# Kernel optimization log

Hardware: AMD Instinct MI355X
Metric: run time of the kernel (lower is better)

## Reference

```python
import jax, jax.numpy as jnp
import numpy as np

DN = ('NCHW', 'OIHW', 'NCHW')

def _conv(x, W, pad):
    return jax.lax.conv_general_dilated(x, W, (1, 1), [(pad, pad), (pad, pad)], dimension_numbers=DN)

def _cbs(x, W, s, b, pad):
    # Conv2d(bias=False) + folded BatchNorm (scale/bias) + SiLU
    y = _conv(x, W, pad) * s[None, :, None, None] + b[None, :, None, None]
    return y * jax.nn.sigmoid(y)

def _l2norm(x):
    n = jnp.sqrt(jnp.sum(x * x, axis=1, keepdims=True))
    return x / jnp.maximum(n, 1e-12)

def setup_inputs() -> dict:
    key = jax.random.key(0)
    ks = jax.random.split(key, 24)
    B, C, H, L, TD, NC = 16, 256, 64, 40, 768, 8
    EMB = (TD + NC * 2) // 2  # 392
    w = lambda k, sh: jax.random.normal(k, sh, jnp.float32) * 0.02
    img = jax.random.normal(ks[0], (B, C, H, H), jnp.float32)
    flang = jax.random.normal(ks[1], (B, L, TD), jnp.float32)
    lengths = jax.random.randint(ks[2], (B, 1), 5, L + 1)
    word_mask = (jnp.arange(L)[None, :] < lengths).astype(jnp.int32)
    return {
        'img': img, 'flang': flang, 'word_mask': word_mask, 'sigma_w': 0.1,
        'W1': w(ks[3], (EMB, TD)), 'b1': w(ks[4], (EMB,)),
        'W2': w(ks[5], (NC * 2, EMB)), 'b2': w(ks[6], (NC * 2,)),
        'Wv': w(ks[7], (C, C, 1, 1)), 'sv': jnp.ones((C,)), 'bv': w(ks[8], (C,)),
        'Wg': w(ks[9], (NC, NC, 1, 1)), 'sg': jnp.ones((NC,)), 'bg': w(ks[10], (NC,)),
        'Wb': w(ks[11], (NC, NC, 1, 1)), 'sb': jnp.ones((NC,)), 'bb': w(ks[12], (NC,)),
        'Wf1': w(ks[13], (C, C, 1, 1)), 'sf1': jnp.ones((C,)), 'bf1': w(ks[14], (C,)),
        'Wf2': w(ks[15], (C, C, 3, 3)), 'sf2': jnp.ones((C,)), 'bf2': w(ks[16], (C,)),
        'Wf3': w(ks[17], (C, C, 1, 1)), 'bf3': w(ks[18], (C,)),
        'Ws': w(ks[19], (NC, C, 3, 3)), 'bs': w(ks[20], (NC,)),
        'add_weight': jnp.zeros((), jnp.float32),
    }

def reference(img, flang, word_mask, sigma_w, W1, b1, W2, b2, Wv, sv, bv,
              Wg, sg, bg, Wb, sb, bb, Wf1, sf1, bf1, Wf2, sf2, bf2,
              Wf3, bf3, Ws, bs, add_weight):
    B, C, H = img.shape[0], img.shape[1], img.shape[2]
    nc = Wg.shape[0]
    map_visu = jnp.tanh(_cbs(img, Wv, sv, bv, 0))
    # ragged masked mean excluding first (CLS) and last (SEP) masked tokens
    m = word_mask.astype(jnp.float32)
    c = jnp.cumsum(m, axis=1)
    tot = c[:, -1:]
    inc = m * ((c > 1) & (c < tot)).astype(jnp.float32)  # [B,L]
    flang_avg = jnp.sum(flang * inc[:, :, None], axis=1) / jnp.sum(inc, axis=1, keepdims=True)
    map_flang = jax.nn.sigmoid((flang_avg @ W1.T + b1) @ W2.T + b2)  # [B,2*nc]
    maps = map_flang.reshape(B, nc, 2)
    sigma_x = sigma_w * H
    sig = _conv(img, Ws, 0) + bs[None, :, None, None]  # [B,nc,H-2,H-2]
    sigma_weight = jax.nn.sigmoid(jnp.mean(sig, axis=(2, 3), keepdims=True))  # [B,nc,1,1]
    sigma_y = sigma_x * sigma_weight
    yc = (maps[:, :, 0] * H).astype(jnp.int32).astype(jnp.float32)[:, :, None, None]
    xc = (maps[:, :, 1] * H).astype(jnp.int32).astype(jnp.float32)[:, :, None, None]
    gy = jnp.arange(H, dtype=jnp.float32)[None, None, :, None]
    gx = jnp.arange(H, dtype=jnp.float32)[None, None, None, :]
    weights = jnp.exp(-((gy - yc) ** 2 / (2.0 * sigma_y ** 2) + (gx - xc) ** 2 / (2.0 * sigma_x ** 2)))  # [B,nc,H,H]
    gamma = jnp.tanh(_cbs(weights, Wg, sg, bg, 0))
    beta = jnp.tanh(_cbs(weights, Wb, sb, bb, 0))
    g = jnp.mean(gamma, axis=1, keepdims=True)
    bmax = jnp.max(beta, axis=1, keepdims=True)
    v_film = _l2norm(g * map_visu + bmax)
    v_film = _cbs(v_film, Wf1, sf1, bf1, 0)
    v_film = _cbs(v_film, Wf2, sf2, bf2, 1)
    v_film = _conv(v_film, Wf3, 0) + bf3[None, :, None, None]
    aw = jnp.tanh(add_weight)
    v_add = (1.0 + aw) * img + (1.0 - aw) * v_film
    return _l2norm(v_add)
```

## Files before the change

### kernel.cpp

```cpp
#include <hip/hip_runtime.h>
#include <hip/hip_bf16.h>


#define DEVFN static __device__ __forceinline__

DEVFN float sigmoidf_(float x) { return 1.f / (1.f + expf(-x)); }
DEVFN float siluf_(float y) { return y / (1.f + expf(-y)); }

typedef __attribute__((ext_vector_type(8))) short bf16x8;
typedef __attribute__((ext_vector_type(4))) float f32x4;

DEVFN unsigned short f2bf_(float f) {
    union { __hip_bfloat16 b; unsigned short u; } cv;
    cv.b = __float2bfloat16(f);
    return cv.u;
}

__global__ void prep_kernel(const float* __restrict__ Wv, const float* __restrict__ Wf1,
                            const float* __restrict__ Wf3, const float* __restrict__ Wf2,
                            short* __restrict__ WvB, short* __restrict__ W1B,
                            short* __restrict__ W3B, short* __restrict__ WB2) {
    int idx = blockIdx.x * 256 + threadIdx.x;
    if (idx < 65536) {
        int j    = idx & 7;
        int lane = (idx >> 3) & 63;
        int coT  = (idx >> 9) & 15;
        int ci32 = (idx >> 13) & 7;
        int co = coT * 16 + (lane & 15);
        int ci = ci32 * 32 + ((lane >> 4) << 3) + j;
        int src = co * 256 + ci;
        WvB[idx] = (short)f2bf_(Wv[src]);
        W1B[idx] = (short)f2bf_(Wf1[src]);
        W3B[idx] = (short)f2bf_(Wf3[src]);
    }
    int o = idx - 65536;
    if (o >= 0 && o < 589824) {
        int j    = o & 7;
        int lane = (o >> 3) & 63;
        int coT  = (o >> 9) & 15;
        int ci32 = (o >> 13) & 7;
        int kk   = o >> 16;
        int co = coT * 16 + (lane & 15);
        int ci = ci32 * 32 + ((lane >> 4) << 3) + j;
        WB2[o] = (short)f2bf_(Wf2[(co * 256 + ci) * 9 + kk]);
    }
}

__global__ void lang_kernel(const float* __restrict__ flang, const int* __restrict__ mask,
                            float* __restrict__ fa) {
    __shared__ float inc[40];
    __shared__ float isum;
    int b = blockIdx.x, t = threadIdx.x;
    if (t == 0) {
        float cum[40];
        float c = 0.f;
        for (int l = 0; l < 40; ++l) { c += (float)mask[b * 40 + l]; cum[l] = c; }
        float tot = c, s = 0.f;
        for (int l = 0; l < 40; ++l) {
            float m = (float)mask[b * 40 + l];
            float v = (cum[l] > 1.f && cum[l] < tot) ? m : 0.f;
            inc[l] = v; s += v;
        }
        isum = s;
    }
    __syncthreads();
    for (int d = t; d < 768; d += 256) {
        float a = 0.f;
        for (int l = 0; l < 40; ++l) a += flang[(size_t)(b * 40 + l) * 768 + d] * inc[l];
        fa[b * 768 + d] = a / isum;
    }
}

__global__ void mlp_kernel(const float* __restrict__ fa_g, const float* __restrict__ W1,
                           const float* __restrict__ b1, const float* __restrict__ W2,
                           const float* __restrict__ b2, float* __restrict__ ycxc) {
    __shared__ float fa[768];
    __shared__ float h[392];
    __shared__ float o[16];
    int b = blockIdx.x, t = threadIdx.x;
    for (int k = t; k < 768; k += 448) fa[k] = fa_g[b * 768 + k];
    __syncthreads();
    if (t < 392) {
        float a = b1[t];
        const float* w = W1 + (size_t)t * 768;
        for (int k = 0; k < 768; ++k) a = fmaf(fa[k], w[k], a);
        h[t] = a;
    }
    __syncthreads();
    if (t < 16) {
        float a = b2[t];
        const float* w = W2 + (size_t)t * 392;
        for (int k = 0; k < 392; ++k) a = fmaf(h[k], w[k], a);
        o[t] = sigmoidf_(a);
    }
    __syncthreads();
    if (t < 8) {
        ycxc[b * 8 + t]       = (float)(int)(o[2 * t] * 64.f);
        ycxc[128 + b * 8 + t] = (float)(int)(o[2 * t + 1] * 64.f);
    }
}

__global__ void wsum_kernel(const float* __restrict__ img, float* __restrict__ S) {
    __shared__ float red[9 * 256];
    int bc = blockIdx.x;
    int t = threadIdx.x;
    float s[9];
#pragma unroll
    for (int k = 0; k < 9; ++k) s[k] = 0.f;
    const float* p = img + (size_t)bc * 4096;
    for (int j = 0; j < 16; ++j) {
        int idx = t + j * 256;
        int y = idx >> 6, x = idx & 63;
        float v = p[idx];
#pragma unroll
        for (int ky = 0; ky < 3; ++ky) {
            if (y < ky || y > ky + 61) continue;
#pragma unroll
            for (int kx = 0; kx < 3; ++kx) {
                if (x < kx || x > kx + 61) continue;
                s[ky * 3 + kx] += v;
            }
        }
    }
#pragma unroll
    for (int k = 0; k < 9; ++k) red[k * 256 + t] = s[k];
    __syncthreads();
    for (int st = 128; st > 0; st >>= 1) {
        if (t < st) {
#pragma unroll
            for (int k = 0; k < 9; ++k) red[k * 256 + t] += red[k * 256 + t + st];
        }
        __syncthreads();
    }
    if (t < 9) S[(size_t)bc * 9 + t] = red[t * 256];
}

__global__ void sigw_kernel(const float* __restrict__ Ws, const float* __restrict__ S,
                            const float* __restrict__ bs, float* __restrict__ sigw) {
    __shared__ float red[8 * 256];
    int b = blockIdx.x, t = threadIdx.x;
    float sv[9];
    const float* Sp = S + (size_t)(b * 256 + t) * 9;
#pragma unroll
    for (int k = 0; k < 9; ++k) sv[k] = Sp[k];
#pragma unroll
    for (int co = 0; co < 8; ++co) {
        const float* wp = Ws + (size_t)(co * 256 + t) * 9;
        float a = 0.f;
#pragma unroll
        for (int k = 0; k < 9; ++k) a = fmaf(wp[k], sv[k], a);
        red[co * 256 + t] = a;
    }
    __syncthreads();
    for (int st = 128; st > 0; st >>= 1) {
        if (t < st) {
#pragma unroll
            for (int co = 0; co < 8; ++co) red[co * 256 + t] += red[co * 256 + t + st];
        }
        __syncthreads();
    }
    if (t < 8) sigw[b * 8 + t] = sigmoidf_(red[t * 256] / 3844.f + bs[t]);
}

__global__ void gauss_kernel(const float* __restrict__ ycxc, const float* __restrict__ sigw,
                             const float* __restrict__ sigma_w,
                             const float* __restrict__ Wg, const float* __restrict__ sg,
                             const float* __restrict__ bg,
                             const float* __restrict__ Wb, const float* __restrict__ sb,
                             const float* __restrict__ bb,
                             float* __restrict__ g, float* __restrict__ bm) {
    int blk = blockIdx.x;
    int b = blk >> 6, y = blk & 63;
    int x = threadIdx.x;
    float sx = sigma_w[0] * 64.f;
    float w[8];
#pragma unroll
    for (int n = 0; n < 8; ++n) {
        float yc = ycxc[b * 8 + n], xc = ycxc[128 + b * 8 + n];
        float sy = sx * sigw[b * 8 + n];
        float dy = (float)y - yc, dx = (float)x - xc;
        w[n] = expf(-(dy * dy / (2.f * sy * sy) + dx * dx / (2.f * sx * sx)));
    }
    float gacc = 0.f, bmax = -3.4e38f;
#pragma unroll
    for (int n = 0; n < 8; ++n) {
        float a1 = 0.f, a2 = 0.f;
#pragma unroll
        for (int m = 0; m < 8; ++m) {
            a1 = fmaf(Wg[n * 8 + m], w[m], a1);
            a2 = fmaf(Wb[n * 8 + m], w[m], a2);
        }
        float ga = tanhf(siluf_(a1 * sg[n] + bg[n]));
        float be = tanhf(siluf_(a2 * sb[n] + bb[n]));
        gacc += ga;
        bmax = fmaxf(bmax, be);
    }
    g[(size_t)(b * 64 + y) * 64 + x] = gacc * 0.125f;
    bm[(size_t)(b * 64 + y) * 64 + x] = bmax;
}

__global__ __launch_bounds__(256) void f01_kernel(
        const float* __restrict__ img, const short* __restrict__ wvb,
        const short* __restrict__ w1b,
        const float* __restrict__ sv, const float* __restrict__ bv,
        const float* __restrict__ s1, const float* __restrict__ b1,
        const float* __restrict__ g, const float* __restrict__ bm,
        __hip_bfloat16* __restrict__ outB) {
    __shared__ __attribute__((aligned(16))) short lA[64 * 264];
    __shared__ float invs[64];
    __shared__ float ls_sv[256], ls_bv[256], ls_s1[256], ls_b1[256];
    __shared__ float ls_g[64], ls_bm[64];
    float* pr = (float*)lA;
    int blk = blockIdx.x, b = blk >> 6, y = blk & 63;
    int t = threadIdx.x, w = t >> 6, lane = t & 63;
    int lx = lane & 15, koct = lane >> 4;

    ls_sv[t] = sv[t]; ls_bv[t] = bv[t];
    ls_s1[t] = s1[t]; ls_b1[t] = b1[t];
    if (t < 64) {
        ls_g[t]  = g[(size_t)(b * 64 + y) * 64 + t];
        ls_bm[t] = bm[(size_t)(b * 64 + y) * 64 + t];
    }

    {
        int x = t & 63, cg = t >> 6;
        const float* ib = img + (size_t)b * 1048576 + y * 64 + x;
#pragma unroll
        for (int c8 = 0; c8 < 8; ++c8) {
            int ci0 = cg * 64 + c8 * 8;
            unsigned short r[8];
#pragma unroll
            for (int j = 0; j < 8; ++j) r[j] = f2bf_(ib[(size_t)(ci0 + j) * 4096]);
            *(uint4*)&lA[x * 264 + ci0] = *(uint4*)r;
        }
    }
    f32x4 acc[4][4];
#pragma unroll
    for (int mi = 0; mi < 4; ++mi)
#pragma unroll
        for (int ni = 0; ni < 4; ++ni) acc[mi][ni] = (f32x4){0.f, 0.f, 0.f, 0.f};
    __syncthreads();

#pragma unroll
    for (int k32 = 0; k32 < 8; ++k32) {
        const short* wp = wvb + (((k32 * 16) + w * 4) * 64 + lane) * 8;
        bf16x8 bfr[4];
#pragma unroll
        for (int ni = 0; ni < 4; ++ni) bfr[ni] = *(const bf16x8*)(wp + ni * 512);
        bf16x8 afr[4];
#pragma unroll
        for (int mi = 0; mi < 4; ++mi)
            afr[mi] = *(const bf16x8*)&lA[(mi * 16 + lx) * 264 + k32 * 32 + koct * 8];
#pragma unroll
        for (int mi = 0; mi < 4; ++mi)
#pragma unroll
            for (int ni = 0; ni < 4; ++ni)
                acc[mi][ni] = __builtin_amdgcn_mfma_f32_16x16x32_bf16(afr[mi], bfr[ni], acc[mi][ni], 0, 0, 0);
    }
    __syncthreads();

#pragma unroll
    for (int mi = 0; mi < 4; ++mi)
#pragma unroll
        for (int rr = 0; rr < 4; ++rr) {
            int x = mi * 16 + koct * 4 + rr;
            float ps = 0.f;
#pragma unroll
            for (int ni = 0; ni < 4; ++ni) {
                int co = w * 64 + ni * 16 + lx;
                float yv = fmaf(acc[mi][ni][rr], ls_sv[co], ls_bv[co]);
                float mvv = tanhf(siluf_(yv));
                float v = fmaf(ls_g[x], mvv, ls_bm[x]);
                acc[mi][ni][rr] = v;
                ps += v * v;
            }
            pr[x * 64 + w * 16 + lx] = ps;
        }
    __syncthreads();
    if (t < 64) {
        float s2 = 0.f;
        for (int q = 0; q < 64; ++q) s2 += pr[t * 64 + q];
        invs[t] = 1.f / fmaxf(sqrtf(s2), 1e-12f);
    }
    __syncthreads();

#pragma unroll
    for (int mi = 0; mi < 4; ++mi)
#pragma unroll
        for (int ni = 0; ni < 4; ++ni) {
            int co = w * 64 + ni * 16 + lx;
#pragma unroll
            for (int rr = 0; rr < 4; ++rr) {
                int x = mi * 16 + koct * 4 + rr;
                lA[x * 264 + co] = (short)f2bf_(acc[mi][ni][rr] * invs[x]);
            }
        }
#pragma unroll
    for (int mi = 0; mi < 4; ++mi)
#pragma unroll
        for (int ni = 0; ni < 4; ++ni) acc[mi][ni] = (f32x4){0.f, 0.f, 0.f, 0.f};
    __syncthreads();

#pragma unroll
    for (int k32 = 0; k32 < 8; ++k32) {
        const short* wp = w1b + (((k32 * 16) + w * 4) * 64 + lane) * 8;
        bf16x8 bfr[4];
#pragma unroll
        for (int ni = 0; ni < 4; ++ni) bfr[ni] = *(const bf16x8*)(wp + ni * 512);
        bf16x8 afr[4];
#pragma unroll
        for (int mi = 0; mi < 4; ++mi)
            afr[mi] = *(const bf16x8*)&lA[(mi * 16 + lx) * 264 + k32 * 32 + koct * 8];
#pragma unroll
        for (int mi = 0; mi < 4; ++mi)
#pragma unroll
            for (int ni = 0; ni < 4; ++ni)
                acc[mi][ni] = __builtin_amdgcn_mfma_f32_16x16x32_bf16(afr[mi], bfr[ni], acc[mi][ni], 0, 0, 0);
    }
    __syncthreads();

#pragma unroll
    for (int mi = 0; mi < 4; ++mi)
#pragma unroll
        for (int ni = 0; ni < 4; ++ni) {
            int co = w * 64 + ni * 16 + lx;
#pragma unroll
            for (int rr = 0; rr < 4; ++rr) {
                int x = mi * 16 + koct * 4 + rr;
                float yv = fmaf(acc[mi][ni][rr], ls_s1[co], ls_b1[co]);
                lA[x * 264 + co] = (short)f2bf_(siluf_(yv));
            }
        }
    __syncthreads();
    unsigned short* og = (unsigned short*)outB + (size_t)(b * 64 + y) * 16384;
#pragma unroll
    for (int it = 0; it < 8; ++it) {
        int e8 = t + it * 256;
        int x2 = e8 >> 5, c8 = e8 & 31;
        *(uint4*)(og + e8 * 8) = *(uint4*)&lA[x2 * 264 + c8 * 8];
    }
}

__global__ __launch_bounds__(256, 2) void conv3x3_mfma(const __hip_bfloat16* __restrict__ xin,
                                                       const short* __restrict__ wb,
                                                       const float* __restrict__ sc,
                                                       const float* __restrict__ bi,
                                                       __hip_bfloat16* __restrict__ outB) {
    __shared__ __attribute__((aligned(16))) short lds[4 * 66 * 72];
    int blk = blockIdx.x;
    int b = blk >> 5, y0 = (blk & 31) * 2;
    int t = threadIdx.x;
    int w = t >> 6, lane = t & 63;
    int lx = lane & 15, koct = lane >> 4;
    const unsigned short* xg = (const unsigned short*)xin + (size_t)b * 1048576;

    f32x4 acc[8][4];
#pragma unroll
    for (int mi = 0; mi < 8; ++mi)
#pragma unroll
        for (int ni = 0; ni < 4; ++ni) acc[mi][ni] = (f32x4){0.f, 0.f, 0.f, 0.f};

    for (int cc = 0; cc < 4; ++cc) {
        __syncthreads();
#pragma unroll
        for (int p = 0; p < 9; ++p) {
            int u = t + p * 256;
            if (u < 2112) {
                int r = u / 528;
                int rem = u - r * 528;
                int xp = rem >> 3, ci8 = rem & 7;
                int ys = y0 + r - 1, xs = xp - 1;
                uint4 v = {0u, 0u, 0u, 0u};
                if (ys >= 0 && ys < 64 && xs >= 0 && xs < 64)
                    v = *(const uint4*)(xg + ((size_t)(ys * 64 + xs) * 256 + cc * 64 + ci8 * 8));
                *(uint4*)&lds[(r * 66 + xp) * 72 + ci8 * 8] = v;
            }
        }
        __syncthreads();
        for (int kk = 0; kk < 9; ++kk) {
            int ky = kk / 3, kx = kk - ky * 3;
#pragma unroll
            for (int k32 = 0; k32 < 2; ++k32) {
                int ci32g = cc * 2 + k32;
                const short* wp = wb + ((((kk * 8 + ci32g) * 16) + w * 4) * 64 + lane) * 8;
                bf16x8 bfr[4];
#pragma unroll
                for (int ni = 0; ni < 4; ++ni)
                    bfr[ni] = *(const bf16x8*)(wp + ni * 512);
                bf16x8 afr[8];
#pragma unroll
                for (int mi = 0; mi < 8; ++mi) {
                    int row = mi >> 2, xb = (mi & 3) * 16;
                    afr[mi] = *(const bf16x8*)&lds[((row + ky) * 66 + xb + lx + kx) * 72 + k32 * 32 + koct * 8];
                }
#pragma unroll
                for (int mi = 0; mi < 8; ++mi)
#pragma unroll
                    for (int ni = 0; ni < 4; ++ni)
                        acc[mi][ni] = __builtin_amdgcn_mfma_f32_16x16x32_bf16(afr[mi], bfr[ni], acc[mi][ni], 0, 0, 0);
            }
        }
    }
#pragma unroll
    for (int r2 = 0; r2 < 2; ++r2) {
        __syncthreads();
#pragma unroll
        for (int mi4 = 0; mi4 < 4; ++mi4) {
            int mi = r2 * 4 + mi4;
#pragma unroll
            for (int ni = 0; ni < 4; ++ni) {
                int co = w * 64 + ni * 16 + lx;
                float s = sc[co], bb2 = bi[co];
#pragma unroll
                for (int rr = 0; rr < 4; ++rr) {
                    int x = mi4 * 16 + koct * 4 + rr;
                    float yv = fmaf(acc[mi][ni][rr], s, bb2);
                    lds[x * 264 + co] = (short)f2bf_(siluf_(yv));
                }
            }
        }
        __syncthreads();
        unsigned short* og = (unsigned short*)outB + (size_t)(b * 64 + y0 + r2) * 16384;
#pragma unroll
        for (int it = 0; it < 8; ++it) {
            int e8 = t + it * 256;
            int x2 = e8 >> 5, c8 = e8 & 31;
            *(uint4*)(og + e8 * 8) = *(uint4*)&lds[x2 * 264 + c8 * 8];
        }
    }
}

__global__ __launch_bounds__(256) void final_mfma(const __hip_bfloat16* __restrict__ inB,
                                                  const short* __restrict__ w3b,
                                                  const float* __restrict__ bf3,
                                                  const float* __restrict__ img,
                                                  const float* __restrict__ addw,
                                                  float* __restrict__ outF) {
    __shared__ __attribute__((aligned(16))) short lA[64 * 264];
    __shared__ float invs[64];
    __shared__ float ls_b[256];
    float* pr = (float*)lA;
    int blk = blockIdx.x, b = blk >> 6, y = blk & 63;
    int t = threadIdx.x, w = t >> 6, lane = t & 63;
    int lx = lane & 15, koct = lane >> 4;
    ls_b[t] = bf3[t];

    const unsigned short* xg = (const unsigned short*)inB + (size_t)(b * 64 + y) * 16384;
#pragma unroll
    for (int it = 0; it < 8; ++it) {
        int e8 = t + it * 256;
        int x2 = e8 >> 5, c8 = e8 & 31;
        *(uint4*)&lA[x2 * 264 + c8 * 8] = *(const uint4*)(xg + e8 * 8);
    }
    f32x4 acc[4][4];
#pragma unroll
    for (int mi = 0; mi < 4; ++mi)
#pragma unroll
        for (int ni = 0; ni < 4; ++ni) acc[mi][ni] = (f32x4){0.f, 0.f, 0.f, 0.f};
    __syncthreads();

#pragma unroll
    for (int k32 = 0; k32 < 8; ++k32) {
        const short* wp = w3b + (((k32 * 16) + w * 4) * 64 + lane) * 8;
        bf16x8 bfr[4];
#pragma unroll
        for (int ni = 0; ni < 4; ++ni) bfr[ni] = *(const bf16x8*)(wp + ni * 512);
        bf16x8 afr[4];
#pragma unroll
        for (int mi = 0; mi < 4; ++mi)
            afr[mi] = *(const bf16x8*)&lA[(mi * 16 + lx) * 264 + k32 * 32 + koct * 8];
#pragma unroll
        for (int mi = 0; mi < 4; ++mi)
#pragma unroll
            for (int ni = 0; ni < 4; ++ni)
                acc[mi][ni] = __builtin_amdgcn_mfma_f32_16x16x32_bf16(afr[mi], bfr[ni], acc[mi][ni], 0, 0, 0);
    }
    __syncthreads();

    float aw = tanhf(addw[0]);
#pragma unroll
    for (int mi = 0; mi < 4; ++mi)
#pragma unroll
        for (int ni = 0; ni < 4; ++ni) {
            int co = w * 64 + ni * 16 + lx;
            const float* ip = img + ((size_t)(b * 256 + co) * 64 + y) * 64 + mi * 16 + koct * 4;
            float4 im = *(const float4*)ip;
            float imv[4] = {im.x, im.y, im.z, im.w};
#pragma unroll
            for (int rr = 0; rr < 4; ++rr) {
                float v = (1.f + aw) * imv[rr] + (1.f - aw) * (acc[mi][ni][rr] + ls_b[co]);
                acc[mi][ni][rr] = v;
            }
        }
#pragma unroll
    for (int mi = 0; mi < 4; ++mi)
#pragma unroll
        for (int rr = 0; rr < 4; ++rr) {
            int x = mi * 16 + koct * 4 + rr;
            float ps = 0.f;
#pragma unroll
            for (int ni = 0; ni < 4; ++ni) ps += acc[mi][ni][rr] * acc[mi][ni][rr];
            pr[x * 64 + w * 16 + lx] = ps;
        }
    __syncthreads();
    if (t < 64) {
        float s2 = 0.f;
        for (int q = 0; q < 64; ++q) s2 += pr[t * 64 + q];
        invs[t] = 1.f / fmaxf(sqrtf(s2), 1e-12f);
    }
    __syncthreads();
#pragma unroll
    for (int mi = 0; mi < 4; ++mi)
#pragma unroll
        for (int ni = 0; ni < 4; ++ni) {
            int co = w * 64 + ni * 16 + lx;
            float r[4];
#pragma unroll
            for (int rr = 0; rr < 4; ++rr) {
                int x = mi * 16 + koct * 4 + rr;
                r[rr] = acc[mi][ni][rr] * invs[x];
            }
            float* op = outF + ((size_t)(b * 256 + co) * 64 + y) * 64 + mi * 16 + koct * 4;
            *(float4*)op = *(float4*)r;
        }
}

extern "C" void kernel_launch(void* const* d_in, const int* in_sizes, int n_in,
                              void* d_out, int out_size, void* d_ws, size_t ws_size,
                              hipStream_t stream) {
    const float* img     = (const float*)d_in[0];
    const float* flang   = (const float*)d_in[1];
    const int*   wmask   = (const int*)d_in[2];
    const float* sigma_w = (const float*)d_in[3];
    const float* W1      = (const float*)d_in[4];
    const float* b1      = (const float*)d_in[5];
    const float* W2      = (const float*)d_in[6];
    const float* b2      = (const float*)d_in[7];
    const float* Wv      = (const float*)d_in[8];
    const float* sv      = (const float*)d_in[9];
    const float* bv      = (const float*)d_in[10];
    const float* Wg      = (const float*)d_in[11];
    const float* sg      = (const float*)d_in[12];
    const float* bg      = (const float*)d_in[13];
    const float* Wb      = (const float*)d_in[14];
    const float* sb      = (const float*)d_in[15];
    const float* bb      = (const float*)d_in[16];
    const float* Wf1     = (const float*)d_in[17];
    const float* sf1     = (const float*)d_in[18];
    const float* bf1     = (const float*)d_in[19];
    const float* Wf2     = (const float*)d_in[20];
    const float* sf2     = (const float*)d_in[21];
    const float* bf2     = (const float*)d_in[22];
    const float* Wf3     = (const float*)d_in[23];
    const float* bf3     = (const float*)d_in[24];
    const float* Ws      = (const float*)d_in[25];
    const float* bs      = (const float*)d_in[26];
    const float* addw    = (const float*)d_in[27];
    float* out = (float*)d_out;
    float* ws  = (float*)d_ws;

    short* WvB  = (short*)ws;
    short* W1B  = (short*)(ws + 32768);
    short* W3B  = (short*)(ws + 65536);
    short* WB2  = (short*)(ws + 98304);
    float* fa   = ws + 393216;
    float* ycxc = ws + 405504;
    float* S    = ws + 405760;
    float* sigw = ws + 442624;
    float* gmap = ws + 442752;
    float* bmap = ws + 508288;
    __hip_bfloat16* bufA = (__hip_bfloat16*)(ws + 573824);
    __hip_bfloat16* bufB = (__hip_bfloat16*)(ws + 8962432);

    prep_kernel<<<2560, 256, 0, stream>>>(Wv, Wf1, Wf3, Wf2, WvB, W1B, W3B, WB2);
    lang_kernel<<<16, 256, 0, stream>>>(flang, wmask, fa);
    mlp_kernel<<<16, 448, 0, stream>>>(fa, W1, b1, W2, b2, ycxc);
    wsum_kernel<<<4096, 256, 0, stream>>>(img, S);
    sigw_kernel<<<16, 256, 0, stream>>>(Ws, S, bs, sigw);
    gauss_kernel<<<1024, 64, 0, stream>>>(ycxc, sigw, sigma_w, Wg, sg, bg, Wb, sb, bb, gmap, bmap);
    f01_kernel<<<1024, 256, 0, stream>>>(img, WvB, W1B, sv, bv, sf1, bf1, gmap, bmap, bufB);
    conv3x3_mfma<<<512, 256, 0, stream>>>(bufB, WB2, sf2, bf2, bufA);
    final_mfma<<<1024, 256, 0, stream>>>(bufA, W3B, bf3, img, addw, out);
}
```

Measured before the change: 430.0 us.

## Prefetch next conv3x3 channel chunk into registers; restructure final kernel epilogue

The 3x3 conv kernel now precomputes load offsets and register-prefetches the next 64-channel input chunk while MFMAs run on the current one, hiding global-load latency behind compute. The final 1x1 kernel stages conv output through LDS as bf16 in a channel-major layout and recomputes the residual-plus-l2norm with coalesced per-pixel img reads and output writes. It also raises its occupancy hint. tanh and SiLU switch to fast-exp approximations. The bf16 staging of the final conv output and the fast math add rounding error, and the extra prefetch registers may raise register pressure.

```diff
diff --git a/kernel.cpp b/kernel.cpp
--- a/kernel.cpp
+++ b/kernel.cpp
@@ -5,7 +5,8 @@
 #define DEVFN static __device__ __forceinline__
 
 DEVFN float sigmoidf_(float x) { return 1.f / (1.f + expf(-x)); }
-DEVFN float siluf_(float y) { return y / (1.f + expf(-y)); }
+DEVFN float siluf_(float y) { return y / (1.f + __expf(-y)); }
+DEVFN float tanh_fast_(float x) { return 1.f - 2.f / (__expf(2.f * x) + 1.f); }
 
 typedef __attribute__((ext_vector_type(8))) short bf16x8;
 typedef __attribute__((ext_vector_type(4))) float f32x4;
@@ -14,6 +15,11 @@
     union { __hip_bfloat16 b; unsigned short u; } cv;
     cv.b = __float2bfloat16(f);
     return cv.u;
+}
+DEVFN float bf2f_(unsigned short u) {
+    union { unsigned short u; __hip_bfloat16 b; } cv;
+    cv.u = u;
+    return __bfloat162float(cv.b);
 }
 
 __global__ void prep_kernel(const float* __restrict__ Wv, const float* __restrict__ Wf1,
@@ -269,7 +275,7 @@
             for (int ni = 0; ni < 4; ++ni) {
                 int co = w * 64 + ni * 16 + lx;
                 float yv = fmaf(acc[mi][ni][rr], ls_sv[co], ls_bv[co]);
-                float mvv = tanhf(siluf_(yv));
+                float mvv = tanh_fast_(siluf_(yv));
                 float v = fmaf(ls_g[x], mvv, ls_bm[x]);
                 acc[mi][ni][rr] = v;
                 ps += v * v;
@@ -354,35 +360,54 @@
     int lx = lane & 15, koct = lane >> 4;
     const unsigned short* xg = (const unsigned short*)xin + (size_t)b * 1048576;
 
+    int goff[9], loff[9];
+    bool uval[9], uin[9];
+#pragma unroll
+    for (int p = 0; p < 9; ++p) {
+        int u = t + p * 256;
+        uval[p] = (u < 2112);
+        int r = u / 528;
+        int rem = u - r * 528;
+        int xp = rem >> 3, ci8 = rem & 7;
+        int ys = y0 + r - 1, xs = xp - 1;
+        uin[p] = uval[p] && ys >= 0 && ys < 64 && xs >= 0 && xs < 64;
+        goff[p] = (ys * 64 + xs) * 256 + ci8 * 8;
+        loff[p] = (r * 66 + xp) * 72 + ci8 * 8;
+    }
+    uint4 pf[9];
+
     f32x4 acc[8][4];
 #pragma unroll
     for (int mi = 0; mi < 8; ++mi)
 #pragma unroll
         for (int ni = 0; ni < 4; ++ni) acc[mi][ni] = (f32x4){0.f, 0.f, 0.f, 0.f};
 
+#pragma unroll
+    for (int p = 0; p < 9; ++p) {
+        uint4 v = {0u, 0u, 0u, 0u};
+        if (uin[p]) v = *(const uint4*)(xg + goff[p]);
+        pf[p] = v;
+    }
+#pragma unroll
+    for (int p = 0; p < 9; ++p)
+        if (uval[p]) *(uint4*)&lds[loff[p]] = pf[p];
+    __syncthreads();
+
     for (int cc = 0; cc < 4; ++cc) {
-        __syncthreads();
-#pragma unroll
-        for (int p = 0; p < 9; ++p) {
-            int u = t + p * 256;
-            if (u < 2112) {
-                int r = u / 528;
-                int rem = u - r * 528;
-                int xp = rem >> 3, ci8 = rem & 7;
-                int ys = y0 + r - 1, xs = xp - 1;
+        if (cc < 3) {
+#pragma unroll
+            for (int p = 0; p < 9; ++p) {
                 uint4 v = {0u, 0u, 0u, 0u};
-                if (ys >= 0 && ys < 64 && xs >= 0 && xs < 64)
-                    v = *(const uint4*)(xg + ((size_t)(ys * 64 + xs) * 256 + cc * 64 + ci8 * 8));
-                *(uint4*)&lds[(r * 66 + xp) * 72 + ci8 * 8] = v;
-            }
-        }
-        __syncthreads();
+                if (uin[p]) v = *(const uint4*)(xg + goff[p] + (cc + 1) * 64);
+                pf[p] = v;
+            }
+        }
+#pragma unroll
         for (int kk = 0; kk < 9; ++kk) {
             int ky = kk / 3, kx = kk - ky * 3;
 #pragma unroll
             for (int k32 = 0; k32 < 2; ++k32) {
-                int ci32g = cc * 2 + k32;
-                const short* wp = wb + ((((kk * 8 + ci32g) * 16) + w * 4) * 64 + lane) * 8;
+                const short* wp = wb + ((((kk * 8 + cc * 2 + k32) * 16) + w * 4) * 64 + lane) * 8;
                 bf16x8 bfr[4];
 #pragma unroll
                 for (int ni = 0; ni < 4; ++ni)
@@ -400,10 +425,16 @@
                         acc[mi][ni] = __builtin_amdgcn_mfma_f32_16x16x32_bf16(afr[mi], bfr[ni], acc[mi][ni], 0, 0, 0);
             }
         }
+        __syncthreads();
+        if (cc < 3) {
+#pragma unroll
+            for (int p = 0; p < 9; ++p)
+                if (uval[p]) *(uint4*)&lds[loff[p]] = pf[p];
+            __syncthreads();
+        }
     }
 #pragma unroll
     for (int r2 = 0; r2 < 2; ++r2) {
-        __syncthreads();
 #pragma unroll
         for (int mi4 = 0; mi4 < 4; ++mi4) {
             int mi = r2 * 4 + mi4;
@@ -427,19 +458,20 @@
             int x2 = e8 >> 5, c8 = e8 & 31;
             *(uint4*)(og + e8 * 8) = *(uint4*)&lds[x2 * 264 + c8 * 8];
         }
-    }
-}
-
-__global__ __launch_bounds__(256) void final_mfma(const __hip_bfloat16* __restrict__ inB,
-                                                  const short* __restrict__ w3b,
-                                                  const float* __restrict__ bf3,
-                                                  const float* __restrict__ img,
-                                                  const float* __restrict__ addw,
-                                                  float* __restrict__ outF) {
+        __syncthreads();
+    }
+}
+
+__global__ __launch_bounds__(256, 4) void final_mfma(const __hip_bfloat16* __restrict__ inB,
+                                                     const short* __restrict__ w3b,
+                                                     const float* __restrict__ bf3,
+                                                     const float* __restrict__ img,
+                                                     const float* __restrict__ addw,
+                                                     float* __restrict__ outF) {
     __shared__ __attribute__((aligned(16))) short lA[64 * 264];
+    __shared__ float pr2[256];
     __shared__ float invs[64];
     __shared__ float ls_b[256];
-    float* pr = (float*)lA;
     int blk = blockIdx.x, b = blk >> 6, y = blk & 63;
     int t = threadIdx.x, w = t >> 6, lane = t & 63;
     int lx = lane & 15, koct = lane >> 4;
@@ -477,52 +509,44 @@
     }
     __syncthreads();
 
-    float aw = tanhf(addw[0]);
 #pragma unroll
     for (int mi = 0; mi < 4; ++mi)
 #pragma unroll
         for (int ni = 0; ni < 4; ++ni) {
             int co = w * 64 + ni * 16 + lx;
-            const float* ip = img + ((size_t)(b * 256 + co) * 64 + y) * 64 + mi * 16 + koct * 4;
-            float4 im = *(const float4*)ip;
-            float imv[4] = {im.x, im.y, im.z, im.w};
-#pragma unroll
-            for (int rr = 0; rr < 4; ++rr) {
-                float v = (1.f + aw) * imv[rr] + (1.f - aw) * (acc[mi][ni][rr] + ls_b[co]);
-                acc[mi][ni][rr] = v;
-            }
-        }
-#pragma unroll
-    for (int mi = 0; mi < 4; ++mi)
-#pragma unroll
-        for (int rr = 0; rr < 4; ++rr) {
-            int x = mi * 16 + koct * 4 + rr;
-            float ps = 0.f;
-#pragma unroll
-            for (int ni = 0; ni < 4; ++ni) ps += acc[mi][ni][rr] * acc[mi][ni][rr];
-            pr[x * 64 + w * 16 + lx] = ps;
-        }
-    __syncthreads();
-    if (t < 64) {
-        float s2 = 0.f;
-        for (int q = 0; q < 64; ++q) s2 += pr[t * 64 + q];
-        invs[t] = 1.f / fmaxf(sqrtf(s2), 1e-12f);
-    }
-    __syncthreads();
-#pragma unroll
-    for (int mi = 0; mi < 4; ++mi)
-#pragma unroll
-        for (int ni = 0; ni < 4; ++ni) {
-            int co = w * 64 + ni * 16 + lx;
-            float r[4];
+            float b3 = ls_b[co];
 #pragma unroll
             for (int rr = 0; rr < 4; ++rr) {
                 int x = mi * 16 + koct * 4 + rr;
-                r[rr] = acc[mi][ni][rr] * invs[x];
-            }
-            float* op = outF + ((size_t)(b * 256 + co) * 64 + y) * 64 + mi * 16 + koct * 4;
-            *(float4*)op = *(float4*)r;
-        }
+                lA[co * 66 + x] = (short)f2bf_(acc[mi][ni][rr] + b3);
+            }
+        }
+    __syncthreads();
+
+    float aw = tanhf(addw[0]);
+    float ca = 1.f + aw, cb = 1.f - aw;
+    int x = t & 63, cg = t >> 6;
+    const float* ip = img + (size_t)b * 1048576 + y * 64 + x;
+    float ss = 0.f;
+#pragma unroll 8
+    for (int j = 0; j < 64; ++j) {
+        int co = cg * 64 + j;
+        float v = fmaf(cb, bf2f_((unsigned short)lA[co * 66 + x]), ca * ip[(size_t)co * 4096]);
+        ss += v * v;
+    }
+    pr2[cg * 64 + x] = ss;
+    __syncthreads();
+    if (t < 64)
+        invs[t] = 1.f / fmaxf(sqrtf(pr2[t] + pr2[64 + t] + pr2[128 + t] + pr2[192 + t]), 1e-12f);
+    __syncthreads();
+    float iv = invs[x];
+    float* op = outF + (size_t)b * 1048576 + y * 64 + x;
+#pragma unroll 8
+    for (int j = 0; j < 64; ++j) {
+        int co = cg * 64 + j;
+        float v = fmaf(cb, bf2f_((unsigned short)lA[co * 66 + x]), ca * ip[(size_t)co * 4096]);
+        op[(size_t)co * 4096] = v * iv;
+    }
 }
 
 extern "C" void kernel_launch(void* const* d_in, const int* in_sizes, int n_in,
```

After: 467.9 us. +8.8%, slower.
